# Performance work log

Measured on AMD Instinct MI355X. Metric: run time of the kernel, lower is better.

Reference implementation:

```python
import jax, jax.numpy as jnp
import numpy as np

IN_FEATURES = 4096
OUT_FEATURES = 4096


def setup_inputs() -> dict:
    key = jax.random.key(0)
    k1, k2 = jax.random.split(key)
    x = jax.random.normal(k1, (4, 2048, IN_FEATURES), dtype=jnp.float32)
    latent_weight = jax.random.normal(k2, (OUT_FEATURES, IN_FEATURES), dtype=jnp.float32) * 0.02
    return {"x": x, "latent_weight": latent_weight}


def _quantize(w):
    # abs-mean scale, ternary {-alpha, 0, alpha} with threshold 0.5*alpha
    alpha = jnp.mean(jnp.abs(w))
    threshold = 0.5 * alpha
    return jnp.where(w > threshold, alpha, jnp.where(w < -threshold, -alpha, jnp.zeros_like(w)))


def reference(x, latent_weight):
    qw = _quantize(latent_weight.astype(jnp.float32))
    # F.linear: x @ qw.T  -> [B, S, out_features]
    out = jnp.einsum('bsi,oi->bso', x.astype(jnp.float32), qw)
    return out.astype(x.dtype)
```

## Files before the change

### kernel.cpp

```cpp
#include <hip/hip_runtime.h>
#include <hip/hip_bf16.h>
#include <stdint.h>

#define M_DIM 8192
#define K_DIM 4096
#define N_DIM 4096

typedef __attribute__((ext_vector_type(8))) short short8;
typedef __attribute__((ext_vector_type(4))) float f32x4;

__device__ __forceinline__ void lds_load16(const ushort* g, ushort* l) {
    __builtin_amdgcn_global_load_lds(
        (const __attribute__((address_space(1))) uint32_t*)g,
        (__attribute__((address_space(3))) uint32_t*)l, 16, 0, 0);
}

__device__ __forceinline__ ushort f2bf_rne(float f) {
    uint32_t u = __float_as_uint(f);
    uint32_t r = (u + 0x7FFFu + ((u >> 16) & 1u)) >> 16;
    return (ushort)r;
}

__global__ void k_abs_partial(const float* __restrict__ w, double* __restrict__ partial) {
    const float4* w4 = (const float4*)w;
    const int n4 = (K_DIM * N_DIM) / 4;
    double s = 0.0;
    for (int i = blockIdx.x * blockDim.x + threadIdx.x; i < n4; i += gridDim.x * blockDim.x) {
        float4 v = w4[i];
        s += (double)fabsf(v.x) + (double)fabsf(v.y) + (double)fabsf(v.z) + (double)fabsf(v.w);
    }
    #pragma unroll
    for (int off = 32; off > 0; off >>= 1) s += __shfl_down(s, off, 64);
    __shared__ double sm[4];
    int lane = threadIdx.x & 63, wv = threadIdx.x >> 6;
    if (lane == 0) sm[wv] = s;
    __syncthreads();
    if (threadIdx.x == 0) partial[blockIdx.x] = sm[0] + sm[1] + sm[2] + sm[3];
}

__global__ void k_alpha(const double* __restrict__ partial, float* __restrict__ alpha_out) {
    double s = 0.0;
    for (int i = threadIdx.x; i < 1024; i += 256) s += partial[i];
    #pragma unroll
    for (int off = 32; off > 0; off >>= 1) s += __shfl_down(s, off, 64);
    __shared__ double sm[4];
    int lane = threadIdx.x & 63, wv = threadIdx.x >> 6;
    if (lane == 0) sm[wv] = s;
    __syncthreads();
    if (threadIdx.x == 0) {
        double total = sm[0] + sm[1] + sm[2] + sm[3];
        alpha_out[0] = (float)(total * (1.0 / 16777216.0));
    }
}

__global__ void k_quant(const float* __restrict__ w, const float* __restrict__ alpha_p,
                        ushort* __restrict__ qw) {
    const float thr = 0.5f * alpha_p[0];
    int i = blockIdx.x * blockDim.x + threadIdx.x;
    float4 v = ((const float4*)w)[i];
    ushort4 q;
    q.x = v.x > thr ? 0x3F80 : (v.x < -thr ? 0xBF80 : 0);
    q.y = v.y > thr ? 0x3F80 : (v.y < -thr ? 0xBF80 : 0);
    q.z = v.z > thr ? 0x3F80 : (v.z < -thr ? 0xBF80 : 0);
    q.w = v.w > thr ? 0x3F80 : (v.w < -thr ? 0xBF80 : 0);
    ((ushort4*)qw)[i] = q;
}

__global__ void k_cast(const float* __restrict__ x, ushort* __restrict__ xb) {
    int i = blockIdx.x * blockDim.x + threadIdx.x;
    float4 v = ((const float4*)x)[i];
    ushort4 o;
    o.x = f2bf_rne(v.x);
    o.y = f2bf_rne(v.y);
    o.z = f2bf_rne(v.z);
    o.w = f2bf_rne(v.w);
    ((ushort4*)xb)[i] = o;
}

#define NT (K_DIM / 64)

#define MFMA16(a, b, c) __builtin_amdgcn_mfma_f32_16x16x32_bf16((a), (b), (c), 0, 0, 0)

__global__ __launch_bounds__(512, 2) void k_gemm(const ushort* __restrict__ A,
                                                 const ushort* __restrict__ B,
                                                 const float* __restrict__ alpha_p,
                                                 float* __restrict__ C) {
    __shared__ __align__(16) ushort lds[65536];

    const int tid = threadIdx.x;
    const int lane = tid & 63;
    const int w = tid >> 6;
    const int wr = w >> 2;
    const int wc = w & 3;
    const int r = lane & 15, q = lane >> 4;

    const int wg = blockIdx.x;
    const int swz = (wg & 7) * 64 + (wg >> 3);
    const int bm = swz >> 4;
    const int bn = swz & 15;

    float alpha = alpha_p[0];
    asm volatile("" :: "v"(alpha));

    const ushort* Abase = A + (size_t)bm * 256 * K_DIM;
    const ushort* Bbase = B + (size_t)bn * 256 * K_DIM;

    const int srow = tid >> 3;
    const int sch = (tid & 7) ^ (srow & 7);

    const int ch0 = q ^ (r & 7);
    const int o0 = r * 64 + ch0 * 8;
    const int o1 = r * 64 + (ch0 ^ 4) * 8;

    f32x4 acc[8][4] = {};

    auto SA = [&](int h, int bb, int tt) {
        const ushort* g = Abase + (size_t)(h * 128 + srow) * K_DIM + tt * 64 + sch * 8;
        ushort* l = lds + bb * 32768 + h * 8192 + tid * 8;
        lds_load16(g, l);
        lds_load16(g + (size_t)64 * K_DIM, l + 4096);
    };
    auto SB = [&](int h, int bb, int tt) {
        const ushort* g = Bbase + (size_t)(h * 128 + srow) * K_DIM + tt * 64 + sch * 8;
        ushort* l = lds + bb * 32768 + 16384 + h * 8192 + tid * 8;
        lds_load16(g, l);
        lds_load16(g + (size_t)64 * K_DIM, l + 4096);
    };

    SA(0, 0, 0); SA(1, 0, 0); SB(0, 0, 0); SB(1, 0, 0);
    SB(0, 1, 1); SB(1, 1, 1);
    asm volatile("s_waitcnt vmcnt(4)" ::: "memory");
    __builtin_amdgcn_s_barrier();

    for (int t = 0; t < NT; ++t) {
        const int b = t & 1;
        const ushort* aL = lds + b * 32768 + wr * 8192;
        const ushort* bL = lds + b * 32768 + 16384 + (wc >> 1) * 8192 + (wc & 1) * 4096;
        short8 am[4][2], b01[2][2], b23[2][2];

        #pragma unroll
        for (int i = 0; i < 4; ++i) {
            am[i][0] = *(const short8*)(aL + i * 1024 + o0);
            am[i][1] = *(const short8*)(aL + i * 1024 + o1);
        }
        #pragma unroll
        for (int j = 0; j < 2; ++j) {
            b01[j][0] = *(const short8*)(bL + j * 1024 + o0);
            b01[j][1] = *(const short8*)(bL + j * 1024 + o1);
        }
        if (t + 1 < NT) SA(0, (t + 1) & 1, t + 1);
        __builtin_amdgcn_s_barrier();
        asm volatile("s_waitcnt lgkmcnt(0)" ::: "memory");
        __builtin_amdgcn_sched_barrier(0);
        __builtin_amdgcn_s_setprio(1);
        #pragma unroll
        for (int i = 0; i < 4; ++i)
            #pragma unroll
            for (int j = 0; j < 2; ++j) {
                acc[i][j] = MFMA16(am[i][0], b01[j][0], acc[i][j]);
                acc[i][j] = MFMA16(am[i][1], b01[j][1], acc[i][j]);
            }
        __builtin_amdgcn_s_setprio(0);
        __builtin_amdgcn_s_barrier();

        #pragma unroll
        for (int j = 0; j < 2; ++j) {
            b23[j][0] = *(const short8*)(bL + (2 + j) * 1024 + o0);
            b23[j][1] = *(const short8*)(bL + (2 + j) * 1024 + o1);
        }
        if (t + 1 < NT) SA(1, (t + 1) & 1, t + 1);
        __builtin_amdgcn_s_barrier();
        asm volatile("s_waitcnt lgkmcnt(0)" ::: "memory");
        __builtin_amdgcn_sched_barrier(0);
        __builtin_amdgcn_s_setprio(1);
        #pragma unroll
        for (int i = 0; i < 4; ++i)
            #pragma unroll
            for (int j = 0; j < 2; ++j) {
                acc[i][2 + j] = MFMA16(am[i][0], b23[j][0], acc[i][2 + j]);
                acc[i][2 + j] = MFMA16(am[i][1], b23[j][1], acc[i][2 + j]);
            }
        __builtin_amdgcn_s_setprio(0);
        __builtin_amdgcn_s_barrier();

        #pragma unroll
        for (int i = 0; i < 4; ++i) {
            am[i][0] = *(const short8*)(aL + (4 + i) * 1024 + o0);
            am[i][1] = *(const short8*)(aL + (4 + i) * 1024 + o1);
        }
        if (t + 2 < NT) SB(0, b, t + 2);
        __builtin_amdgcn_s_barrier();
        asm volatile("s_waitcnt lgkmcnt(0)" ::: "memory");
        __builtin_amdgcn_sched_barrier(0);
        __builtin_amdgcn_s_setprio(1);
        #pragma unroll
        for (int i = 0; i < 4; ++i)
            #pragma unroll
            for (int j = 0; j < 2; ++j) {
                acc[4 + i][2 + j] = MFMA16(am[i][0], b23[j][0], acc[4 + i][2 + j]);
                acc[4 + i][2 + j] = MFMA16(am[i][1], b23[j][1], acc[4 + i][2 + j]);
            }
        __builtin_amdgcn_s_setprio(0);
        __builtin_amdgcn_s_barrier();

        if (t + 2 < NT) SB(1, b, t + 2);
        __builtin_amdgcn_s_barrier();
        __builtin_amdgcn_s_setprio(1);
        #pragma unroll
        for (int i = 0; i < 4; ++i)
            #pragma unroll
            for (int j = 0; j < 2; ++j) {
                acc[4 + i][j] = MFMA16(am[i][0], b01[j][0], acc[4 + i][j]);
                acc[4 + i][j] = MFMA16(am[i][1], b01[j][1], acc[4 + i][j]);
            }
        __builtin_amdgcn_s_setprio(0);
        if (t + 2 < NT)       asm volatile("s_waitcnt vmcnt(4)" ::: "memory");
        else if (t + 2 == NT) asm volatile("s_waitcnt vmcnt(0)" ::: "memory");
        __builtin_amdgcn_s_barrier();
    }

    const int row0 = bm * 256 + wr * 128 + q * 4;
    const int col0 = bn * 256 + wc * 64 + r;
    #pragma unroll
    for (int i = 0; i < 8; ++i)
        #pragma unroll
        for (int j = 0; j < 4; ++j)
            #pragma unroll
            for (int v = 0; v < 4; ++v)
                C[(size_t)(row0 + i * 16 + v) * N_DIM + col0 + j * 16] = alpha * acc[i][j][v];
}

extern "C" void kernel_launch(void* const* d_in, const int* in_sizes, int n_in,
                              void* d_out, int out_size, void* d_ws, size_t ws_size,
                              hipStream_t stream) {
    const float* x = (const float*)d_in[0];
    const float* w = (const float*)d_in[1];
    float* out = (float*)d_out;

    char* ws = (char*)d_ws;
    double* partial = (double*)ws;
    float* alpha = (float*)(ws + 8192);
    ushort* qw = (ushort*)(ws + 16384);
    ushort* xb = (ushort*)(ws + 16384 + (size_t)K_DIM * N_DIM * 2);

    k_abs_partial<<<1024, 256, 0, stream>>>(w, partial);
    k_alpha<<<1, 256, 0, stream>>>(partial, alpha);
    k_quant<<<(K_DIM * N_DIM / 4) / 256, 256, 0, stream>>>(w, alpha, qw);
    k_cast<<<(M_DIM * K_DIM / 4) / 256, 256, 0, stream>>>(x, xb);

    k_gemm<<<512, 512, 0, stream>>>(xb, qw, alpha, out);
}
```

Measured before the change: 490.2 us.

## Fuse x cast into abs-sum kernel and reshape GEMM prefetch schedule

Folds the fp32-to-bf16 cast of x into the weight abs-sum reduction kernel, so one grid-stride launch does both and a separate launch goes away. The quantize kernel becomes grid-stride and writes 8 bf16 values per store. In the GEMM, the A tiles for the next step are now prefetched two iterations ahead like B, with loads grouped into larger batches and one barrier removed. The deeper A prefetch needs both LDS buffers in flight at once, and the new wait-count values must match the reordered loads.

```diff
diff --git a/kernel.cpp b/kernel.cpp
--- a/kernel.cpp
+++ b/kernel.cpp
@@ -21,11 +21,14 @@
     return (ushort)r;
 }
 
-__global__ void k_abs_partial(const float* __restrict__ w, double* __restrict__ partial) {
+__global__ void k_prep(const float* __restrict__ w, double* __restrict__ partial,
+                       const float* __restrict__ x, ushort* __restrict__ xb) {
+    const int nth = gridDim.x * blockDim.x;
+    const int gtid = blockIdx.x * blockDim.x + threadIdx.x;
+
     const float4* w4 = (const float4*)w;
-    const int n4 = (K_DIM * N_DIM) / 4;
     double s = 0.0;
-    for (int i = blockIdx.x * blockDim.x + threadIdx.x; i < n4; i += gridDim.x * blockDim.x) {
+    for (int i = gtid; i < (K_DIM * N_DIM) / 4; i += nth) {
         float4 v = w4[i];
         s += (double)fabsf(v.x) + (double)fabsf(v.y) + (double)fabsf(v.z) + (double)fabsf(v.w);
     }
@@ -36,11 +39,23 @@
     if (lane == 0) sm[wv] = s;
     __syncthreads();
     if (threadIdx.x == 0) partial[blockIdx.x] = sm[0] + sm[1] + sm[2] + sm[3];
+
+    const float4* x4 = (const float4*)x;
+    ushort4* xb4 = (ushort4*)xb;
+    for (int i = gtid; i < (M_DIM * K_DIM) / 4; i += nth) {
+        float4 v = x4[i];
+        ushort4 o;
+        o.x = f2bf_rne(v.x);
+        o.y = f2bf_rne(v.y);
+        o.z = f2bf_rne(v.z);
+        o.w = f2bf_rne(v.w);
+        xb4[i] = o;
+    }
 }
 
 __global__ void k_alpha(const double* __restrict__ partial, float* __restrict__ alpha_out) {
     double s = 0.0;
-    for (int i = threadIdx.x; i < 1024; i += 256) s += partial[i];
+    for (int i = threadIdx.x; i < 2048; i += 256) s += partial[i];
     #pragma unroll
     for (int off = 32; off > 0; off >>= 1) s += __shfl_down(s, off, 64);
     __shared__ double sm[4];
@@ -56,25 +71,23 @@
 __global__ void k_quant(const float* __restrict__ w, const float* __restrict__ alpha_p,
                         ushort* __restrict__ qw) {
     const float thr = 0.5f * alpha_p[0];
-    int i = blockIdx.x * blockDim.x + threadIdx.x;
-    float4 v = ((const float4*)w)[i];
-    ushort4 q;
-    q.x = v.x > thr ? 0x3F80 : (v.x < -thr ? 0xBF80 : 0);
-    q.y = v.y > thr ? 0x3F80 : (v.y < -thr ? 0xBF80 : 0);
-    q.z = v.z > thr ? 0x3F80 : (v.z < -thr ? 0xBF80 : 0);
-    q.w = v.w > thr ? 0x3F80 : (v.w < -thr ? 0xBF80 : 0);
-    ((ushort4*)qw)[i] = q;
-}
-
-__global__ void k_cast(const float* __restrict__ x, ushort* __restrict__ xb) {
-    int i = blockIdx.x * blockDim.x + threadIdx.x;
-    float4 v = ((const float4*)x)[i];
-    ushort4 o;
-    o.x = f2bf_rne(v.x);
-    o.y = f2bf_rne(v.y);
-    o.z = f2bf_rne(v.z);
-    o.w = f2bf_rne(v.w);
-    ((ushort4*)xb)[i] = o;
+    const int nth = gridDim.x * blockDim.x;
+    const int gtid = blockIdx.x * blockDim.x + threadIdx.x;
+    const float4* w4 = (const float4*)w;
+    short8* q8 = (short8*)qw;
+    for (int i = gtid; i < (K_DIM * N_DIM) / 8; i += nth) {
+        float4 a = w4[2 * i], b = w4[2 * i + 1];
+        short8 o;
+        o[0] = a.x > thr ? (short)0x3F80 : (a.x < -thr ? (short)0xBF80 : (short)0);
+        o[1] = a.y > thr ? (short)0x3F80 : (a.y < -thr ? (short)0xBF80 : (short)0);
+        o[2] = a.z > thr ? (short)0x3F80 : (a.z < -thr ? (short)0xBF80 : (short)0);
+        o[3] = a.w > thr ? (short)0x3F80 : (a.w < -thr ? (short)0xBF80 : (short)0);
+        o[4] = b.x > thr ? (short)0x3F80 : (b.x < -thr ? (short)0xBF80 : (short)0);
+        o[5] = b.y > thr ? (short)0x3F80 : (b.y < -thr ? (short)0xBF80 : (short)0);
+        o[6] = b.z > thr ? (short)0x3F80 : (b.z < -thr ? (short)0xBF80 : (short)0);
+        o[7] = b.w > thr ? (short)0x3F80 : (b.w < -thr ? (short)0xBF80 : (short)0);
+        q8[i] = o;
+    }
 }
 
 #define NT (K_DIM / 64)
@@ -129,7 +142,8 @@
 
     SA(0, 0, 0); SA(1, 0, 0); SB(0, 0, 0); SB(1, 0, 0);
     SB(0, 1, 1); SB(1, 1, 1);
-    asm volatile("s_waitcnt vmcnt(4)" ::: "memory");
+    SA(0, 1, 1); SA(1, 1, 1);
+    asm volatile("s_waitcnt vmcnt(8)" ::: "memory");
     __builtin_amdgcn_s_barrier();
 
     for (int t = 0; t < NT; ++t) {
@@ -148,7 +162,7 @@
             b01[j][0] = *(const short8*)(bL + j * 1024 + o0);
             b01[j][1] = *(const short8*)(bL + j * 1024 + o1);
         }
-        if (t + 1 < NT) SA(0, (t + 1) & 1, t + 1);
+        asm volatile("s_waitcnt lgkmcnt(8)" ::: "memory");
         __builtin_amdgcn_s_barrier();
         asm volatile("s_waitcnt lgkmcnt(0)" ::: "memory");
         __builtin_amdgcn_sched_barrier(0);
@@ -168,7 +182,6 @@
             b23[j][0] = *(const short8*)(bL + (2 + j) * 1024 + o0);
             b23[j][1] = *(const short8*)(bL + (2 + j) * 1024 + o1);
         }
-        if (t + 1 < NT) SA(1, (t + 1) & 1, t + 1);
         __builtin_amdgcn_s_barrier();
         asm volatile("s_waitcnt lgkmcnt(0)" ::: "memory");
         __builtin_amdgcn_sched_barrier(0);
@@ -188,7 +201,7 @@
             am[i][0] = *(const short8*)(aL + (4 + i) * 1024 + o0);
             am[i][1] = *(const short8*)(aL + (4 + i) * 1024 + o1);
         }
-        if (t + 2 < NT) SB(0, b, t + 2);
+        if (t + 2 < NT) { SB(0, b, t + 2); SB(1, b, t + 2); }
         __builtin_amdgcn_s_barrier();
         asm volatile("s_waitcnt lgkmcnt(0)" ::: "memory");
         __builtin_amdgcn_sched_barrier(0);
@@ -203,8 +216,7 @@
         __builtin_amdgcn_s_setprio(0);
         __builtin_amdgcn_s_barrier();
 
-        if (t + 2 < NT) SB(1, b, t + 2);
-        __builtin_amdgcn_s_barrier();
+        if (t + 2 < NT) { SA(0, b, t + 2); SA(1, b, t + 2); }
         __builtin_amdgcn_s_setprio(1);
         #pragma unroll
         for (int i = 0; i < 4; ++i)
@@ -214,8 +226,8 @@
                 acc[4 + i][j] = MFMA16(am[i][1], b01[j][1], acc[4 + i][j]);
             }
         __builtin_amdgcn_s_setprio(0);
-        if (t + 2 < NT)       asm volatile("s_waitcnt vmcnt(4)" ::: "memory");
-        else if (t + 2 == NT) asm volatile("s_waitcnt vmcnt(0)" ::: "memory");
+        if (t + 2 < NT) asm volatile("s_waitcnt vmcnt(8)" ::: "memory");
+        else            asm volatile("s_waitcnt vmcnt(0)" ::: "memory");
         __builtin_amdgcn_s_barrier();
     }
 
@@ -239,14 +251,13 @@
 
     char* ws = (char*)d_ws;
     double* partial = (double*)ws;
-    float* alpha = (float*)(ws + 8192);
-    ushort* qw = (ushort*)(ws + 16384);
-    ushort* xb = (ushort*)(ws + 16384 + (size_t)K_DIM * N_DIM * 2);
-
-    k_abs_partial<<<1024, 256, 0, stream>>>(w, partial);
+    float* alpha = (float*)(ws + 16384);
+    ushort* qw = (ushort*)(ws + 32768);
+    ushort* xb = (ushort*)(ws + 32768 + (size_t)K_DIM * N_DIM * 2);
+
+    k_prep<<<2048, 256, 0, stream>>>(w, partial, x, xb);
     k_alpha<<<1, 256, 0, stream>>>(partial, alpha);
-    k_quant<<<(K_DIM * N_DIM / 4) / 256, 256, 0, stream>>>(w, alpha, qw);
-    k_cast<<<(M_DIM * K_DIM / 4) / 256, 256, 0, stream>>>(x, xb);
+    k_quant<<<2048, 256, 0, stream>>>(w, alpha, qw);
 
     k_gemm<<<512, 512, 0, stream>>>(xb, qw, alpha, out);
 }
```

New measurement: 509.7 us. +4.0%, slower.
